# Kernel optimization log

Hardware: AMD Instinct MI355X
Metric: run time of the kernel (lower is better)

Reference implementation:

```python
import jax, jax.numpy as jnp
from jax import lax
import numpy as np

EPS = 1e-5

def _conv(x, w, pad):
    return lax.conv_general_dilated(x, w, (1, 1), ((pad, pad), (pad, pad)),
                                    dimension_numbers=('NCHW', 'OIHW', 'NCHW'))

def _bn_relu(x, g, b, m, v):
    scale = g * lax.rsqrt(v + EPS)
    shift = b - m * scale
    return jax.nn.relu(x * scale[:, None, None] + shift[:, None, None])

def _pam(x, kw, kb, vw, vb, gamma):
    # x: [B,C,H,W]; key/query share the same 1x1 conv (as in source)
    B, C, H, W = x.shape
    q = (_conv(x, kw, 0) + kb[:, None, None]).reshape(B, -1, H * W)      # [B,C/8,HW]
    attn = jax.nn.softmax(jnp.einsum('bci,bcj->bij', q, q), axis=-1)     # [B,HW,HW]
    v = (_conv(x, vw, 0) + vb[:, None, None]).reshape(B, C, H * W)       # [B,C,HW]
    out = jnp.einsum('bcj,bij->bci', v, attn).reshape(B, C, H, W)        # value @ attn^T
    return gamma * out + x

def _cam(x, gamma):
    B, C, H, W = x.shape
    f = x.reshape(B, C, H * W)
    energy = jnp.einsum('bcm,bdm->bcd', f, f)                            # [B,C,C]
    attn = jax.nn.softmax(jnp.max(energy, -1, keepdims=True) - energy, axis=-1)
    out = jnp.einsum('bcd,bdm->bcm', attn, f).reshape(B, C, H, W)
    return gamma * out + x

def setup_inputs() -> dict:
    key = jax.random.key(0)
    ks = iter(jax.random.split(key, 40))
    Cin, Cm, Cout = 512, 128, 64  # in_channels, in_channels//ratio, out_channels
    Ck = Cm // 8                  # PAM key channels
    n = lambda shape, s: jax.random.normal(next(ks), shape, jnp.float32) * s
    def bn(c):
        return dict(g=n((c,), 1.0) * 0 + 1.0 + n((c,), 0.1),
                    b=n((c,), 0.1), m=n((c,), 0.1), v=jnp.abs(n((c,), 0.5)) + 0.5)
    bn11, bn12, bn21, bn22 = bn(Cm), bn(Cm), bn(Cm), bn(Cm)
    return {
        'x': jax.random.normal(next(ks), (4, Cin, 64, 64), jnp.float32),
        'w11': n((Cm, Cin, 3, 3), 0.02), 'g11': bn11['g'], 'b11': bn11['b'], 'm11': bn11['m'], 'v11': bn11['v'],
        'w12': n((Cm, Cin, 3, 3), 0.02), 'g12': bn12['g'], 'b12': bn12['b'], 'm12': bn12['m'], 'v12': bn12['v'],
        'pam_kw': n((Ck, Cm, 1, 1), 0.05), 'pam_kb': n((Ck,), 0.02),
        'pam_vw': n((Cm, Cm, 1, 1), 0.05), 'pam_vb': n((Cm,), 0.02),
        'pam_gamma': n((1,), 0.1), 'cam_gamma': n((1,), 0.1),
        'w21': n((Cm, Cm, 3, 3), 0.03), 'g21': bn21['g'], 'b21': bn21['b'], 'm21': bn21['m'], 'v21': bn21['v'],
        'w22': n((Cm, Cm, 3, 3), 0.03), 'g22': bn22['g'], 'b22': bn22['b'], 'm22': bn22['m'], 'v22': bn22['v'],
        'w31': n((Cout, Cm, 1, 1), 0.05), 'b31': n((Cout,), 0.02),
        'w32': n((Cout, Cm, 1, 1), 0.05), 'b32': n((Cout,), 0.02),
        'w4':  n((Cout, Cm, 1, 1), 0.05), 'b4':  n((Cout,), 0.02),
    }

def reference(x, w11, g11, b11, m11, v11, w12, g12, b12, m12, v12,
              pam_kw, pam_kb, pam_vw, pam_vb, pam_gamma, cam_gamma,
              w21, g21, b21, m21, v21, w22, g22, b22, m22, v22,
              w31, b31, w32, b32, w4, b4):
    # Dropout2d(p=0.1) is identity at eval time; BatchNorm uses running stats.
    feat1 = _bn_relu(_conv(x, w11, 1), g11, b11, m11, v11)
    pa_feat = _pam(feat1, pam_kw, pam_kb, pam_vw, pam_vb, pam_gamma)
    pa_conv = _bn_relu(_conv(pa_feat, w21, 1), g21, b21, m21, v21)
    pa_out = _conv(pa_conv, w31, 0) + b31[:, None, None]

    feat2 = _bn_relu(_conv(x, w12, 1), g12, b12, m12, v12)
    ca_feat = _cam(feat2, cam_gamma)
    ca_conv = _bn_relu(_conv(ca_feat, w22, 1), g22, b22, m22, v22)
    ca_out = _conv(ca_conv, w32, 0) + b32[:, None, None]

    feat_sum = pa_conv + ca_conv
    feat_sum_out = _conv(feat_sum, w4, 0) + b4[:, None, None]
    return jnp.stack([pa_out, ca_out, feat_sum_out])  # [3,B,Cout,H,W]
```

## Files before the change

kernel.cpp:

```cpp
#include <hip/hip_runtime.h>
#include <stdint.h>

typedef unsigned short u16;
typedef unsigned int   u32;
typedef unsigned long long u64;
typedef __attribute__((ext_vector_type(8))) short bf16x8;
typedef __attribute__((ext_vector_type(4))) float f32x4;

#define DEV static __device__ __forceinline__

DEV float b2f(u16 u){ u32 x = ((u32)u) << 16; float f; __builtin_memcpy(&f, &x, 4); return f; }
DEV u16 f2b(float f){ u32 x; __builtin_memcpy(&x, &f, 4); return (u16)((x + 0x7fffu + ((x >> 16) & 1u)) >> 16); }
DEV float ldf(const void* p, int i, int flg){
  return flg ? b2f(((const u16*)p)[i]) : ((const float*)p)[i];
}
DEV void gload_lds16(const u16* g, u16* l){
  __builtin_amdgcn_global_load_lds((const __attribute__((address_space(1))) void*)g,
                                   (__attribute__((address_space(3))) void*)l, 16, 0, 0);
}

static constexpr int HW   = 4096;
static constexpr int PPIX = 4356;

__global__ void k_detect(const u32* __restrict__ x, int* __restrict__ flag)
{
  __shared__ int cnt;
  if (threadIdx.x == 0) cnt = 0;
  __syncthreads();
  const u32 w  = x[threadIdx.x];
  const u32 eb = (w >> 7) & 0xFFu;
  if (eb >= 100u && eb <= 150u) atomicAdd(&cnt, 1);
  __syncthreads();
  if (threadIdx.x == 0) *flag = (cnt > 384) ? 1 : 0;
}

__global__ void k_cvt(const void* __restrict__ src, const int* __restrict__ flagp,
                      u16* __restrict__ dst, int n)
{
  const int i = (blockIdx.x * 256 + threadIdx.x) << 2;
  if (i >= n) return;
  u64 ov;
  if (*flagp){
    ov = ((const u64*)src)[i >> 2];
  } else {
    const float4 f = ((const float4*)src)[i >> 2];
    const u16 a0 = f2b(f.x), a1 = f2b(f.y), a2 = f2b(f.z), a3 = f2b(f.w);
    ov = (u64)a0 | ((u64)a1 << 16) | ((u64)a2 << 32) | ((u64)a3 << 48);
  }
  ((u64*)dst)[i >> 2] = ov;
}

__global__ void k_prep(
    const void* g0,const void* b0,const void* m0,const void* v0,
    const void* g1,const void* b1,const void* m1,const void* v1,
    const void* g2,const void* b2,const void* m2,const void* v2,
    const void* g3,const void* b3,const void* m3,const void* v3,
    const int* __restrict__ flagp, float* scale, float* shift)
{
  const int t = threadIdx.x;
  if (t >= 512) return;
  const int flg = *flagp;
  const int set = t >> 7, c = t & 127;
  const void *gp,*bp,*mp,*vp;
  if      (set == 0){gp=g0;bp=b0;mp=m0;vp=v0;}
  else if (set == 1){gp=g1;bp=b1;mp=m1;vp=v1;}
  else if (set == 2){gp=g2;bp=b2;mp=m2;vp=v2;}
  else              {gp=g3;bp=b3;mp=m3;vp=v3;}
  const float sc = ldf(gp,c,flg) * rsqrtf(ldf(vp,c,flg) + 1e-5f);
  scale[t] = sc;
  shift[t] = ldf(bp,c,flg) - ldf(mp,c,flg) * sc;
}

__global__ void k_reorder_cvt(const void* __restrict__ win, const int* __restrict__ flagp,
                              u16* __restrict__ wout, int cin)
{
  const int idx = blockIdx.x * 256 + threadIdx.x;
  const int flg = *flagp;
  const int n9 = cin * 9;
  const int co = idx / n9;
  const int rem = idx - co * n9;
  const int ci = rem / 9;
  const int rs = rem - ci * 9;
  const u16 v = flg ? ((const u16*)win)[idx] : f2b(((const float*)win)[idx]);
  wout[co * n9 + rs * cin + ci] = v;
}

template<int C_>
__global__ void k_halo(u16* __restrict__ buf)
{
  const int tid = blockIdx.x * 256 + threadIdx.x;
  const int e  = tid * 8;
  const int cc = e % C_;
  int rem = e / C_;
  const int hp = rem % 260;
  const int b  = rem / 260;
  int pix;
  if      (hp < 66)  pix = hp;
  else if (hp < 132) pix = 65 * 66 + (hp - 66);
  else if (hp < 196) pix = (hp - 132 + 1) * 66;
  else               pix = (hp - 196 + 1) * 66 + 65;
  uint4 z; z.x = 0; z.y = 0; z.z = 0; z.w = 0;
  *(uint4*)(buf + ((size_t)b * PPIX + pix) * C_ + cc) = z;
}

__global__ __launch_bounds__(256) void k_xT(
    const void* __restrict__ src, const int* __restrict__ flagp, u16* __restrict__ dst)
{
  const int t = threadIdx.x, wave = t >> 6, lane = t & 63;
  const int pb = blockIdx.x & 31, ct = (blockIdx.x >> 5) & 7, b = blockIdx.x >> 8;
  const int c  = ct * 64 + lane;
  const int p0 = pb * 128 + wave * 32;
  const size_t sbase = ((size_t)(b * 512) + c) * 4096 + p0;

  u16 vals[32];
  if (*flagp){
    const u16* s = (const u16*)src + sbase;
    #pragma unroll
    for (int k = 0; k < 4; ++k){
      uint4 v = *(const uint4*)(s + k * 8);
      __builtin_memcpy(&vals[k * 8], &v, 16);
    }
  } else {
    const float* s = (const float*)src + sbase;
    #pragma unroll
    for (int k = 0; k < 8; ++k){
      float4 v = *(const float4*)(s + k * 4);
      vals[k*4+0] = f2b(v.x); vals[k*4+1] = f2b(v.y);
      vals[k*4+2] = f2b(v.z); vals[k*4+3] = f2b(v.w);
    }
  }
  const int hrow = (p0 >> 6) * 66 + (p0 & 63) + 67;
  u16* d = dst + ((size_t)b * PPIX + hrow) * 512 + c;
  #pragma unroll
  for (int k = 0; k < 32; ++k) d[(size_t)k * 512] = vals[k];
}

template<int CIN_, bool PADOUT_, bool DUALB_>
__global__ __launch_bounds__(256, 1) void k_cgemm(
    const u16* __restrict__ xA, const u16* __restrict__ xB,
    const u16* __restrict__ wA, const u16* __restrict__ wB,
    const float* __restrict__ scale, const float* __restrict__ shift,
    u16* __restrict__ outA, u16* __restrict__ outBp, u16* __restrict__ outB2)
{
  constexpr int K9   = 9 * CIN_;
  constexpr int NCH  = CIN_ / 64;
  constexpr int OPIX = PADOUT_ ? PPIX : 4096;

  __shared__ __align__(16) u16 At[128 * 64];
  __shared__ __align__(16) u16 Bt[128 * 64];

  const int t = threadIdx.x;
  const int w = t >> 6, lane = t & 63;
  const int l16 = lane & 15, quad = lane >> 4;

  const int cid = blockIdx.x >> 7;
  const int t7  = blockIdx.x & 127;
  const int b   = t7 >> 5;
  const int p0  = (t7 & 31) << 7;

  const u16* xin = cid ? xB : xA;
  const u16* wK  = cid ? wB : wA;
  const float* sc = scale + cid * 128;
  const float* sh = shift + cid * 128;

  const int rowS = t >> 3;
  const int sw   = ((t & 7) ^ (rowS & 7)) << 3;

  const u16* gA[4]; const u16* gB[4];
  u16* lA[4]; u16* lB[4];
  #pragma unroll
  for (int k = 0; k < 4; ++k){
    const int rA = k * 32 + rowS;
    gA[k] = wK + (size_t)rA * K9 + sw;
    const int px = p0 + k * 32 + rowS;
    const int h = px >> 6, wc = px & 63;
    gB[k] = xin + ((size_t)b * PPIX + h * 66 + wc) * CIN_ + sw;
    lA[k] = At + k * 2048 + w * 512;
    lB[k] = Bt + k * 2048 + w * 512;
  }

  f32x4 acc[4][4];
  #pragma unroll
  for (int mi = 0; mi < 4; ++mi)
    #pragma unroll
    for (int ni = 0; ni < 4; ++ni){
      acc[mi][ni][0]=0.f; acc[mi][ni][1]=0.f; acc[mi][ni][2]=0.f; acc[mi][ni][3]=0.f;
    }

  const int wc4 = (w >> 1) << 6;
  const int wp4 = (w & 1) << 6;

  #pragma unroll 1
  for (int tap = 0; tap < 9; ++tap){
    const int tb = (tap / 3) * 66 + (tap % 3);
    #pragma unroll 1
    for (int cc = 0; cc < NCH; ++cc){
      const int offA = tap * CIN_ + cc * 64;
      const int offB = tb  * CIN_ + cc * 64;
      #pragma unroll
      for (int k = 0; k < 4; ++k){
        gload_lds16(gA[k] + offA, lA[k]);
        gload_lds16(gB[k] + offB, lB[k]);
      }
      __syncthreads();
      #pragma unroll
      for (int ks = 0; ks < 2; ++ks){
        bf16x8 af[4], bf[4];
        const int col = ((ks * 4 + quad) ^ (l16 & 7)) << 3;
        #pragma unroll
        for (int mi = 0; mi < 4; ++mi)
          af[mi] = *(const bf16x8*)(At + ((wc4 + mi * 16 + l16) << 6) + col);
        #pragma unroll
        for (int ni = 0; ni < 4; ++ni)
          bf[ni] = *(const bf16x8*)(Bt + ((wp4 + ni * 16 + l16) << 6) + col);
        #pragma unroll
        for (int mi = 0; mi < 4; ++mi)
          #pragma unroll
          for (int ni = 0; ni < 4; ++ni)
            acc[mi][ni] = __builtin_amdgcn_mfma_f32_16x16x32_bf16(af[mi], bf[ni], acc[mi][ni], 0, 0, 0);
      }
      __syncthreads();
    }
  }

  u16* outp = cid ? outBp : outA;
  #pragma unroll
  for (int mi = 0; mi < 4; ++mi){
    #pragma unroll
    for (int ni = 0; ni < 4; ++ni){
      const int px = p0 + wp4 + ni * 16 + l16;
      const int opix = PADOUT_ ? ((px >> 6) * 66 + (px & 63) + 67) : px;
      const int co4 = wc4 + mi * 16 + quad * 4;
      u16 pk[4];
      #pragma unroll
      for (int rr = 0; rr < 4; ++rr)
        pk[rr] = f2b(fmaxf(acc[mi][ni][rr] * sc[co4 + rr] + sh[co4 + rr], 0.f));
      u64 pkv; __builtin_memcpy(&pkv, pk, 8);
      *(u64*)(outp + ((size_t)b * OPIX + opix) * 128 + co4) = pkv;
      if constexpr (DUALB_){
        if (cid){
          #pragma unroll
          for (int rr = 0; rr < 4; ++rr)
            outB2[((size_t)(b * 128) + co4 + rr) * 4096 + px] = pk[rr];
        }
      }
    }
  }
}

template<int CIN_, int CO_, int EPI_, bool SUM2_, bool PADIN_, bool PADOUT_, bool WPB_>
__global__ __launch_bounds__(256) void k_convT(
    const u16* __restrict__ xin, const u16* __restrict__ xin2,
    const u16* __restrict__ wK,
    const void* __restrict__ bias, const int* __restrict__ flagp,
    u16* __restrict__ outB, float* __restrict__ outF)
{
  constexpr int K    = CIN_;
  constexpr int MT   = CO_ / 16;
  constexpr int IPIX = PADIN_ ? PPIX : 4096;
  constexpr int OPIX = PADOUT_ ? PPIX : 4096;

  const int tid  = threadIdx.x;
  const int wave = tid >> 6;
  const int lane = tid & 63;
  const int l16  = lane & 15;
  const int quad = lane >> 4;

  int tile = blockIdx.x * 4 + wave;
  const int nt = tile & 255; tile >>= 8;
  const int mt = tile % MT;
  const int b  = tile / MT;

  const int p = nt * 16 + l16;
  const int h = p >> 6, wc = p & 63;

  const u16* wrow = wK + (WPB_ ? (size_t)b * CO_ * K : 0)
                       + (size_t)(mt * 16 + l16) * K + quad * 8;
  const u16* xb   = xin + (size_t)b * IPIX * CIN_ + quad * 8;

  f32x4 acc = {0.f, 0.f, 0.f, 0.f};

  const int poff = PADIN_ ? (h * 66 + wc + 67) : p;
  const u16* xrs = xb + (size_t)poff * CIN_;
  const u16* xrs2 = nullptr;
  if constexpr (SUM2_) xrs2 = xin2 + (size_t)b * IPIX * CIN_ + quad * 8 + (size_t)poff * CIN_;
  #pragma unroll
  for (int ci0 = 0; ci0 < CIN_; ci0 += 32){
    bf16x8 af = *(const bf16x8*)(wrow + ci0);
    bf16x8 bf;
    if constexpr (SUM2_){
      bf16x8 b1 = *(const bf16x8*)(xrs + ci0);
      bf16x8 b2 = *(const bf16x8*)(xrs2 + ci0);
      #pragma unroll
      for (int j = 0; j < 8; ++j)
        bf[j] = (short)f2b(b2f((u16)b1[j]) + b2f((u16)b2[j]));
    } else {
      bf = *(const bf16x8*)(xrs + ci0);
    }
    acc = __builtin_amdgcn_mfma_f32_16x16x32_bf16(af, bf, acc, 0, 0, 0);
  }

  const int flg = *flagp;

  if constexpr (EPI_ == 4){
    #pragma unroll
    for (int rr = 0; rr < 4; ++rr){
      const int co = quad * 4 + rr;
      const float vv = acc[rr] + ldf(bias, co, flg);
      const u16 hb = f2b(vv);
      const float lo = vv - b2f(hb);
      const size_t qaddr = ((size_t)b * 4096 + p) * 16 + co;
      outB[qaddr] = hb;
      ((u16*)outF)[qaddr] = f2b(lo);
    }
  } else if constexpr (EPI_ == 6){
    const float g = ldf(bias, 0, flg);
    const int opix = PADOUT_ ? (h * 66 + wc + 67) : p;
    const int co4 = mt * 16 + quad * 4;
    const size_t addr = ((size_t)b * OPIX + opix) * CO_ + co4;
    u64 rv = *(const u64*)(xin2 + (size_t)b * OPIX * CO_ + (size_t)opix * CO_ + co4);
    u16 rk[4]; __builtin_memcpy(rk, &rv, 8);
    u16 pk[4];
    #pragma unroll
    for (int rr = 0; rr < 4; ++rr)
      pk[rr] = f2b(g * acc[rr] + b2f(rk[rr]));
    u64 pkv; __builtin_memcpy(&pkv, pk, 8);
    *(u64*)(outB + addr) = pkv;
  } else {
    #pragma unroll
    for (int rr = 0; rr < 4; ++rr){
      const int co = mt * 16 + quad * 4 + rr;
      const float vv = acc[rr] + ldf(bias, co, flg);
      const size_t addr = ((size_t)(b * CO_) + co) * 4096 + p;
      if constexpr (EPI_ == 2) outB[addr] = f2b(vv);
      else { if (flg) outB[addr] = f2b(vv); else outF[addr] = vv; }
    }
  }
}

__global__ __launch_bounds__(256) void k_pam_flash(
    const u16* __restrict__ qTh, const u16* __restrict__ qTl,
    const u16* __restrict__ v,
    u16* __restrict__ po, float* __restrict__ pm, float* __restrict__ pl)
{
  __shared__ __align__(16) u16 vls[1024 * 8];
  __shared__ __align__(16) u16 pls[4][128 * 8];

  const int t    = threadIdx.x;
  const int wave = t >> 6, lane = t & 63;
  const int l16  = lane & 15, quad = lane >> 4;

  const int bid = blockIdx.x;
  const int js  = bid & 3, it = (bid >> 2) & 63, b = bid >> 8;
  const int i0  = it * 64;
  const int jbase = js * 1024;

  const u16* qTbh = qTh + ((size_t)b * 4096) * 16;
  const u16* qTbl = qTl + ((size_t)b * 4096) * 16;
  const u16* vb   = v + ((size_t)b * 128) * 4096;

  bf16x8 af_hl, af_h0 = {};
  {
    const int i = i0 + wave * 16 + l16;
    const u16* src = ((quad < 2) ? qTbh : qTbl) + (size_t)i * 16 + (quad & 1) * 8;
    *(uint4*)&af_hl = *(const uint4*)src;
    if (quad < 2) af_h0 = af_hl;
  }

  const u16* vsrcB[4];
  u16* vdstB[4];
  #pragma unroll
  for (int k = 0; k < 4; ++k){
    const int p = t + 256 * k;
    const int c  = ((p >> 7) << 4) | (p & 15);
    const int jl = ((p >> 6) & 1) * 32 + ((p >> 4) & 3) * 8;
    vsrcB[k] = vb + (size_t)c * 4096 + jbase + jl;
    vdstB[k] = vls + ((size_t)(wave * 64 + 256 * k)) * 8;
  }

  f32x4 oacc[8];
  #pragma unroll
  for (int cs = 0; cs < 8; ++cs){ oacc[cs][0]=0.f; oacc[cs][1]=0.f; oacc[cs][2]=0.f; oacc[cs][3]=0.f; }
  float m_run[4], l_run[4];
  #pragma unroll
  for (int r = 0; r < 4; ++r){ m_run[r] = -1e30f; l_run[r] = 0.f; }

  for (int ch = 0; ch < 16; ++ch){
    const int j0 = ch * 64;
    __syncthreads();
    #pragma unroll
    for (int k = 0; k < 4; ++k)
      gload_lds16(vsrcB[k] + j0, vdstB[k]);

    f32x4 sacc[4];
    #pragma unroll
    for (int ns = 0; ns < 4; ++ns){
      const int j = jbase + j0 + ns * 16 + l16;
      bf16x8 b_hh, b_ll;
      *(uint4*)&b_hh = *(const uint4*)(qTbh + (size_t)j * 16 + (quad & 1) * 8);
      *(uint4*)&b_ll = *(const uint4*)(qTbl + (size_t)j * 16 + (quad & 1) * 8);
      f32x4 z = {0.f, 0.f, 0.f, 0.f};
      z = __builtin_amdgcn_mfma_f32_16x16x32_bf16(af_hl, b_hh, z, 0, 0, 0);
      z = __builtin_amdgcn_mfma_f32_16x16x32_bf16(af_h0, b_ll, z, 0, 0, 0);
      sacc[ns] = z;
    }
    float pv[4][4];
    #pragma unroll
    for (int r = 0; r < 4; ++r){
      float mx = fmaxf(fmaxf(sacc[0][r], sacc[1][r]), fmaxf(sacc[2][r], sacc[3][r]));
      mx = fmaxf(mx, __shfl_xor(mx, 1));
      mx = fmaxf(mx, __shfl_xor(mx, 2));
      mx = fmaxf(mx, __shfl_xor(mx, 4));
      mx = fmaxf(mx, __shfl_xor(mx, 8));
      const float mnew  = fmaxf(m_run[r], mx);
      const float alpha = __expf(m_run[r] - mnew);
      m_run[r] = mnew;
      float rs = 0.f;
      #pragma unroll
      for (int ns = 0; ns < 4; ++ns){
        pv[ns][r] = __expf(sacc[ns][r] - mnew);
        rs += pv[ns][r];
      }
      rs += __shfl_xor(rs, 1); rs += __shfl_xor(rs, 2);
      rs += __shfl_xor(rs, 4); rs += __shfl_xor(rs, 8);
      l_run[r] = l_run[r] * alpha + rs;
      #pragma unroll
      for (int cs = 0; cs < 8; ++cs) oacc[cs][r] *= alpha;
    }
    #pragma unroll
    for (int ns = 0; ns < 4; ++ns){
      const int ks = ns >> 1;
      const int qp = (ns * 2 + (l16 >> 3)) & 3;
      #pragma unroll
      for (int r = 0; r < 4; ++r)
        pls[wave][(ks * 64 + qp * 16 + quad * 4 + r) * 8 + (l16 & 7)] = f2b(pv[ns][r]);
    }
    __syncthreads();
    #pragma unroll
    for (int ks = 0; ks < 2; ++ks){
      bf16x8 pf = *(const bf16x8*)(pls[wave] + ((ks * 64 + lane) << 3));
      #pragma unroll
      for (int cs = 0; cs < 8; ++cs){
        bf16x8 vf = *(const bf16x8*)(vls + (((cs * 2 + ks) * 64 + lane) << 3));
        oacc[cs] = __builtin_amdgcn_mfma_f32_16x16x32_bf16(pf, vf, oacc[cs], 0, 0, 0);
      }
    }
  }

  u16* pob = po + (size_t)bid * 64 * 128;
  #pragma unroll
  for (int cs = 0; cs < 8; ++cs)
    #pragma unroll
    for (int r = 0; r < 4; ++r)
      pob[(wave * 16 + quad * 4 + r) * 128 + cs * 16 + l16] = f2b(oacc[cs][r]);
  if (l16 == 0){
    #pragma unroll
    for (int r = 0; r < 4; ++r){
      pm[(size_t)bid * 64 + wave * 16 + quad * 4 + r] = m_run[r];
      pl[(size_t)bid * 64 + wave * 16 + quad * 4 + r] = l_run[r];
    }
  }
}

__global__ __launch_bounds__(256) void k_pam_comb2(
    const u16* __restrict__ po, const float* __restrict__ pm, const float* __restrict__ pl,
    const void* __restrict__ gptr, const int* __restrict__ flagp,
    u16* __restrict__ featT)
{
  __shared__ float wgt[4][64];
  const int t  = threadIdx.x;
  const int it = blockIdx.x & 63, b = blockIdx.x >> 6;
  const int base = (b * 64 + it) * 4;
  if (t < 64){
    const float m0 = pm[(size_t)(base+0)*64 + t];
    const float m1 = pm[(size_t)(base+1)*64 + t];
    const float m2 = pm[(size_t)(base+2)*64 + t];
    const float m3 = pm[(size_t)(base+3)*64 + t];
    const float M  = fmaxf(fmaxf(m0, m1), fmaxf(m2, m3));
    const float e0 = __expf(m0 - M), e1 = __expf(m1 - M);
    const float e2 = __expf(m2 - M), e3 = __expf(m3 - M);
    const float L  = pl[(size_t)(base+0)*64+t]*e0 + pl[(size_t)(base+1)*64+t]*e1
                   + pl[(size_t)(base+2)*64+t]*e2 + pl[(size_t)(base+3)*64+t]*e3;
    const float li = 1.0f / L;
    wgt[0][t] = e0*li; wgt[1][t] = e1*li; wgt[2][t] = e2*li; wgt[3][t] = e3*li;
  }
  __syncthreads();
  const float g = ldf(gptr, 0, *flagp);
  const int c = t & 127, ih = t >> 7;
  const int i0 = it * 64;
  for (int st = 0; st < 32; ++st){
    const int il = ih + st * 2;
    float acc = 0.f;
    #pragma unroll
    for (int s = 0; s < 4; ++s)
      acc += wgt[s][il] * b2f(po[((size_t)(base+s)*64 + il)*128 + c]);
    const int i = i0 + il;
    const int pix = (i >> 6) * 66 + (i & 63) + 67;
    u16* addr = featT + ((size_t)b * PPIX + pix) * 128 + c;
    *addr = f2b(g * acc + b2f(*addr));
  }
}

__global__ __launch_bounds__(128) void k_cam_attn(
    const u16* __restrict__ f, u16* __restrict__ attnc)
{
  __shared__ float fc[4096];
  __shared__ float red[128];
  const int d = threadIdx.x;
  const int c = blockIdx.x & 127, b = blockIdx.x >> 7;
  const u16* fb   = f + (size_t)b * 128 * HW;
  const u16* rowc = fb + (size_t)c * HW;
  for (int mi = d; mi < 4096; mi += 128) fc[mi] = b2f(rowc[mi]);
  __syncthreads();

  const u16* rowd = fb + (size_t)d * HW;
  float e = 0.f;
  for (int mm = 0; mm < 4096; mm += 8){
    const uint4 xv = *(const uint4*)(rowd + mm);
    const u16* px = (const u16*)&xv;
    #pragma unroll
    for (int k = 0; k < 8; ++k) e += fc[mm + k] * b2f(px[k]);
  }
  red[d] = e;
  __syncthreads();
  for (int st = 64; st > 0; st >>= 1){
    if (d < st) red[d] = fminf(red[d], red[d + st]);
    __syncthreads();
  }
  const float emin = red[0];
  __syncthreads();
  const float pd = __expf(emin - e);
  red[d] = pd;
  __syncthreads();
  for (int st = 64; st > 0; st >>= 1){
    if (d < st) red[d] += red[d + st];
    __syncthreads();
  }
  attnc[((size_t)b * 128 + c) * 128 + d] = f2b(pd / red[0]);
}

extern "C" void kernel_launch(void* const* d_in, const int* in_sizes, int n_in,
                              void* d_out, int out_size, void* d_ws, size_t ws_size,
                              hipStream_t stream)
{
  (void)in_sizes; (void)n_in; (void)out_size; (void)ws_size;

  const void* x    = d_in[0];
  const void* w11  = d_in[1];
  const void* g11  = d_in[2];
  const void* b11  = d_in[3];
  const void* m11  = d_in[4];
  const void* v11  = d_in[5];
  const void* w12  = d_in[6];
  const void* g12  = d_in[7];
  const void* b12  = d_in[8];
  const void* m12  = d_in[9];
  const void* v12  = d_in[10];
  const void* kw   = d_in[11];
  const void* kb   = d_in[12];
  const void* vw   = d_in[13];
  const void* vb   = d_in[14];
  const void* pgam = d_in[15];
  const void* cgam = d_in[16];
  const void* w21  = d_in[17];
  const void* g21  = d_in[18];
  const void* b21  = d_in[19];
  const void* m21  = d_in[20];
  const void* v21  = d_in[21];
  const void* w22  = d_in[22];
  const void* g22  = d_in[23];
  const void* b22  = d_in[24];
  const void* m22  = d_in[25];
  const void* v22  = d_in[26];
  const void* w31  = d_in[27];
  const void* b31  = d_in[28];
  const void* w32  = d_in[29];
  const void* b32  = d_in[30];
  const void* w4   = d_in[31];
  const void* b4   = d_in[32];

  char* wsb = (char*)d_ws;
  size_t off = 0;
  auto alloc = [&](size_t bytes) -> void* {
    void* pp = wsb + off;
    off += (bytes + 255) & ~(size_t)255;
    return pp;
  };
  u16*   xT      = (u16*)alloc((size_t)4 * PPIX * 512 * 2);
  u16*   feat1T  = (u16*)alloc((size_t)4 * PPIX * 128 * 2);
  u16*   feat2T  = (u16*)alloc((size_t)4 * PPIX * 128 * 2);
  u16*   feat2cm = (u16*)alloc((size_t)4 * 128 * HW * 2);
  u16*   cafeatT = (u16*)alloc((size_t)4 * PPIX * 128 * 2);
  u16*   vbuf    = (u16*)alloc((size_t)4 * 128 * HW * 2);
  u16*   caconvT = (u16*)alloc((size_t)4 * HW * 128 * 2);
  u16*   qTh     = (u16*)alloc((size_t)4 * HW * 16 * 2);
  u16*   qTl     = (u16*)alloc((size_t)4 * HW * 16 * 2);
  float* pm      = (float*)alloc((size_t)1024 * 64 * 4);
  float* pl      = (float*)alloc((size_t)1024 * 64 * 4);
  u16*   attnc   = (u16*)alloc((size_t)4 * 128 * 128 * 2);
  float* scale   = (float*)alloc(512 * 4);
  float* shift   = (float*)alloc(512 * 4);
  u16*   w11r    = (u16*)alloc((size_t)128 * 4608 * 2);
  u16*   w12r    = (u16*)alloc((size_t)128 * 4608 * 2);
  u16*   w21r    = (u16*)alloc((size_t)128 * 1152 * 2);
  u16*   w22r    = (u16*)alloc((size_t)128 * 1152 * 2);
  u16*   kwb     = (u16*)alloc((size_t)16 * 128 * 2);
  u16*   vwb     = (u16*)alloc((size_t)128 * 128 * 2);
  u16*   w31b    = (u16*)alloc((size_t)64 * 128 * 2);
  u16*   w32b    = (u16*)alloc((size_t)64 * 128 * 2);
  u16*   w4b     = (u16*)alloc((size_t)64 * 128 * 2);
  int*   flag    = (int*)alloc(256);
  u16*   po      = xT;

  k_detect<<<1, 512, 0, stream>>>((const u32*)x, flag);
  k_prep<<<1, 512, 0, stream>>>(g11,b11,m11,v11, g12,b12,m12,v12,
                                g21,b21,m21,v21, g22,b22,m22,v22, flag, scale, shift);
  k_halo<512><<<260, 256, 0, stream>>>(xT);
  k_halo<128><<<65, 256, 0, stream>>>(feat1T);
  k_halo<128><<<65, 256, 0, stream>>>(cafeatT);
  k_xT<<<1024, 256, 0, stream>>>(x, flag, xT);
  k_reorder_cvt<<<2304, 256, 0, stream>>>(w11, flag, w11r, 512);
  k_reorder_cvt<<<2304, 256, 0, stream>>>(w12, flag, w12r, 512);
  k_reorder_cvt<<<576, 256, 0, stream>>>(w21, flag, w21r, 128);
  k_reorder_cvt<<<576, 256, 0, stream>>>(w22, flag, w22r, 128);
  k_cvt<<<2, 256, 0, stream>>>(kw, flag, kwb, 16 * 128);
  k_cvt<<<16, 256, 0, stream>>>(vw, flag, vwb, 128 * 128);
  k_cvt<<<8, 256, 0, stream>>>(w31, flag, w31b, 64 * 128);
  k_cvt<<<8, 256, 0, stream>>>(w32, flag, w32b, 64 * 128);
  k_cvt<<<8, 256, 0, stream>>>(w4, flag, w4b, 64 * 128);

  k_cgemm<512, true, true><<<256, 256, 0, stream>>>(
      xT, xT, w11r, w12r, scale, shift, feat1T, feat2T, feat2cm);

  k_convT<128,16,4,false,true,false,false><<<256,256,0,stream>>>(
      feat1T, nullptr, kwb, kb, flag, qTh, (float*)qTl);
  k_convT<128,128,2,false,true,false,false><<<2048,256,0,stream>>>(
      feat1T, nullptr, vwb, vb, flag, vbuf, nullptr);
  k_pam_flash<<<1024, 256, 0, stream>>>(qTh, qTl, vbuf, po, pm, pl);
  k_pam_comb2<<<256, 256, 0, stream>>>(po, pm, pl, pgam, flag, feat1T);

  k_cam_attn<<<512, 128, 0, stream>>>(feat2cm, attnc);
  k_convT<128,128,6,false,true,true,true><<<2048,256,0,stream>>>(
      feat2T, feat2T, attnc, cgam, flag, cafeatT, nullptr);

  k_cgemm<128, false, false><<<256, 256, 0, stream>>>(
      feat1T, cafeatT, w21r, w22r, scale + 256, shift + 256, vbuf, caconvT, nullptr);

  const size_t SEC = (size_t)4 * 64 * HW;
  u16*   outB = (u16*)d_out;
  float* outF = (float*)d_out;
  k_convT<128,64,3,false,false,false,false><<<1024,256,0,stream>>>(
      vbuf,    nullptr, w31b, b31, flag, outB,           outF);
  k_convT<128,64,3,false,false,false,false><<<1024,256,0,stream>>>(
      caconvT, nullptr, w32b, b32, flag, outB + SEC,     outF + SEC);
  k_convT<128,64,3,true ,false,false,false><<<1024,256,0,stream>>>(
      vbuf,    caconvT, w4b,  b4,  flag, outB + 2 * SEC, outF + 2 * SEC);
}
```

Before: 480.2 us.

## Merge prep launches, precompute PAM row max, MFMA-based CAM energy

Merges the detect, convert, reorder and halo kernels into fewer launches so fewer small kernels are dispatched. In PAM flash attention, a first pass computes the exact row max from the high-half scores, so the online-softmax rescaling, shuffles and running-sum reduction go away; row sums are now accumulated with an extra MFMA against a ones vector. CAM energy moves from a scalar per-row dot-product kernel to an MFMA tile kernel with far fewer blocks. The row max is approximated from the high part only and probabilities are truncated to bf16, which may shift numerics slightly, and the extra max pass adds Q reads.

```diff
diff --git a/kernel.cpp b/kernel.cpp
--- a/kernel.cpp
+++ b/kernel.cpp
@@ -11,6 +11,7 @@
 
 DEV float b2f(u16 u){ u32 x = ((u32)u) << 16; float f; __builtin_memcpy(&f, &x, 4); return f; }
 DEV u16 f2b(float f){ u32 x; __builtin_memcpy(&x, &f, 4); return (u16)((x + 0x7fffu + ((x >> 16) & 1u)) >> 16); }
+DEV u16 f2b_trunc(float f){ u32 x; __builtin_memcpy(&x, &f, 4); return (u16)(x >> 16); }
 DEV float ldf(const void* p, int i, int flg){
   return flg ? b2f(((const u16*)p)[i]) : ((const float*)p)[i];
 }
@@ -22,44 +23,26 @@
 static constexpr int HW   = 4096;
 static constexpr int PPIX = 4356;
 
-__global__ void k_detect(const u32* __restrict__ x, int* __restrict__ flag)
-{
-  __shared__ int cnt;
-  if (threadIdx.x == 0) cnt = 0;
-  __syncthreads();
-  const u32 w  = x[threadIdx.x];
-  const u32 eb = (w >> 7) & 0xFFu;
-  if (eb >= 100u && eb <= 150u) atomicAdd(&cnt, 1);
-  __syncthreads();
-  if (threadIdx.x == 0) *flag = (cnt > 384) ? 1 : 0;
-}
-
-__global__ void k_cvt(const void* __restrict__ src, const int* __restrict__ flagp,
-                      u16* __restrict__ dst, int n)
-{
-  const int i = (blockIdx.x * 256 + threadIdx.x) << 2;
-  if (i >= n) return;
-  u64 ov;
-  if (*flagp){
-    ov = ((const u64*)src)[i >> 2];
-  } else {
-    const float4 f = ((const float4*)src)[i >> 2];
-    const u16 a0 = f2b(f.x), a1 = f2b(f.y), a2 = f2b(f.z), a3 = f2b(f.w);
-    ov = (u64)a0 | ((u64)a1 << 16) | ((u64)a2 << 32) | ((u64)a3 << 48);
-  }
-  ((u64*)dst)[i >> 2] = ov;
-}
-
 __global__ void k_prep(
+    const u32* __restrict__ x,
     const void* g0,const void* b0,const void* m0,const void* v0,
     const void* g1,const void* b1,const void* m1,const void* v1,
     const void* g2,const void* b2,const void* m2,const void* v2,
     const void* g3,const void* b3,const void* m3,const void* v3,
-    const int* __restrict__ flagp, float* scale, float* shift)
-{
+    int* __restrict__ flag, float* scale, float* shift)
+{
+  __shared__ int cnt;
+  __shared__ int sflag;
   const int t = threadIdx.x;
-  if (t >= 512) return;
-  const int flg = *flagp;
+  if (t == 0) cnt = 0;
+  __syncthreads();
+  const u32 w  = x[t];
+  const u32 eb = (w >> 7) & 0xFFu;
+  if (eb >= 100u && eb <= 150u) atomicAdd(&cnt, 1);
+  __syncthreads();
+  if (t == 0){ sflag = (cnt > 384) ? 1 : 0; *flag = sflag; }
+  __syncthreads();
+  const int flg = sflag;
   const int set = t >> 7, c = t & 127;
   const void *gp,*bp,*mp,*vp;
   if      (set == 0){gp=g0;bp=b0;mp=m0;vp=v0;}
@@ -71,10 +54,43 @@
   shift[t] = ldf(bp,c,flg) - ldf(mp,c,flg) * sc;
 }
 
-__global__ void k_reorder_cvt(const void* __restrict__ win, const int* __restrict__ flagp,
-                              u16* __restrict__ wout, int cin)
-{
-  const int idx = blockIdx.x * 256 + threadIdx.x;
+__global__ void k_cvt5(
+    const void* s0,const void* s1,const void* s2,const void* s3,const void* s4,
+    const int* __restrict__ flagp,
+    u16* d0,u16* d1,u16* d2,u16* d3,u16* d4)
+{
+  const int g = blockIdx.x * 256 + threadIdx.x;
+  if (g >= 10752) return;
+  const void* s; u16* d; int base;
+  if      (g < 512) { s=s0; d=d0; base=0;    }
+  else if (g < 4608){ s=s1; d=d1; base=512;  }
+  else if (g < 6656){ s=s2; d=d2; base=4608; }
+  else if (g < 8704){ s=s3; d=d3; base=6656; }
+  else              { s=s4; d=d4; base=8704; }
+  const int i = g - base;
+  u64 ov;
+  if (*flagp){
+    ov = ((const u64*)s)[i];
+  } else {
+    const float4 f = ((const float4*)s)[i];
+    const u16 a0 = f2b(f.x), a1 = f2b(f.y), a2 = f2b(f.z), a3 = f2b(f.w);
+    ov = (u64)a0 | ((u64)a1 << 16) | ((u64)a2 << 32) | ((u64)a3 << 48);
+  }
+  ((u64*)d)[i] = ov;
+}
+
+__global__ void k_reorder4(
+    const void* w11,const void* w12,const void* w21,const void* w22,
+    const int* __restrict__ flagp,
+    u16* o11,u16* o12,u16* o21,u16* o22)
+{
+  int blk = blockIdx.x;
+  const void* win; u16* wout; int cin;
+  if      (blk < 2304){ win=w11; wout=o11; cin=512; }
+  else if (blk < 4608){ win=w12; wout=o12; cin=512; blk-=2304; }
+  else if (blk < 5184){ win=w21; wout=o21; cin=128; blk-=4608; }
+  else                { win=w22; wout=o22; cin=128; blk-=5184; }
+  const int idx = blk * 256 + threadIdx.x;
   const int flg = *flagp;
   const int n9 = cin * 9;
   const int co = idx / n9;
@@ -85,13 +101,17 @@
   wout[co * n9 + rs * cin + ci] = v;
 }
 
-template<int C_>
-__global__ void k_halo(u16* __restrict__ buf)
-{
-  const int tid = blockIdx.x * 256 + threadIdx.x;
+__global__ void k_halo3(u16* __restrict__ xT, u16* __restrict__ f1, u16* __restrict__ cf)
+{
+  int blk = blockIdx.x;
+  u16* buf; int cmask, csh;
+  if      (blk < 260){ buf = xT; cmask = 511; csh = 9; }
+  else if (blk < 325){ buf = f1; cmask = 127; csh = 7; blk -= 260; }
+  else               { buf = cf; cmask = 127; csh = 7; blk -= 325; }
+  const int tid = blk * 256 + threadIdx.x;
   const int e  = tid * 8;
-  const int cc = e % C_;
-  int rem = e / C_;
+  const int cc = e & cmask;
+  const int rem = e >> csh;
   const int hp = rem % 260;
   const int b  = rem / 260;
   int pix;
@@ -100,7 +120,7 @@
   else if (hp < 196) pix = (hp - 132 + 1) * 66;
   else               pix = (hp - 196 + 1) * 66 + 65;
   uint4 z; z.x = 0; z.y = 0; z.z = 0; z.w = 0;
-  *(uint4*)(buf + ((size_t)b * PPIX + pix) * C_ + cc) = z;
+  *(uint4*)(buf + ((size_t)b * PPIX + pix) * (cmask + 1) + cc) = z;
 }
 
 __global__ __launch_bounds__(256) void k_xT(
@@ -367,6 +387,31 @@
     if (quad < 2) af_h0 = af_hl;
   }
 
+  float mloc[4] = {-3e38f, -3e38f, -3e38f, -3e38f};
+  #pragma unroll 1
+  for (int ch = 0; ch < 16; ++ch){
+    #pragma unroll
+    for (int ns = 0; ns < 4; ++ns){
+      const int j = jbase + ch * 64 + ns * 16 + l16;
+      bf16x8 bh;
+      *(uint4*)&bh = *(const uint4*)(qTbh + (size_t)j * 16 + (quad & 1) * 8);
+      f32x4 z = {0.f, 0.f, 0.f, 0.f};
+      z = __builtin_amdgcn_mfma_f32_16x16x32_bf16(af_hl, bh, z, 0, 0, 0);
+      #pragma unroll
+      for (int r = 0; r < 4; ++r) mloc[r] = fmaxf(mloc[r], z[r]);
+    }
+  }
+  float mrow[4];
+  #pragma unroll
+  for (int r = 0; r < 4; ++r){
+    float mm = mloc[r];
+    mm = fmaxf(mm, __shfl_xor(mm, 1));
+    mm = fmaxf(mm, __shfl_xor(mm, 2));
+    mm = fmaxf(mm, __shfl_xor(mm, 4));
+    mm = fmaxf(mm, __shfl_xor(mm, 8));
+    mrow[r] = mm;
+  }
+
   const u16* vsrcB[4];
   u16* vdstB[4];
   #pragma unroll
@@ -378,13 +423,15 @@
     vdstB[k] = vls + ((size_t)(wave * 64 + 256 * k)) * 8;
   }
 
+  const short oneb = (short)0x3F80;
+  const bf16x8 vones = {oneb,oneb,oneb,oneb,oneb,oneb,oneb,oneb};
+
   f32x4 oacc[8];
   #pragma unroll
   for (int cs = 0; cs < 8; ++cs){ oacc[cs][0]=0.f; oacc[cs][1]=0.f; oacc[cs][2]=0.f; oacc[cs][3]=0.f; }
-  float m_run[4], l_run[4];
-  #pragma unroll
-  for (int r = 0; r < 4; ++r){ m_run[r] = -1e30f; l_run[r] = 0.f; }
-
+  f32x4 lacc = {0.f, 0.f, 0.f, 0.f};
+
+  #pragma unroll 1
   for (int ch = 0; ch < 16; ++ch){
     const int j0 = ch * 64;
     __syncthreads();
@@ -392,48 +439,22 @@
     for (int k = 0; k < 4; ++k)
       gload_lds16(vsrcB[k] + j0, vdstB[k]);
 
-    f32x4 sacc[4];
     #pragma unroll
     for (int ns = 0; ns < 4; ++ns){
       const int j = jbase + j0 + ns * 16 + l16;
-      bf16x8 b_hh, b_ll;
-      *(uint4*)&b_hh = *(const uint4*)(qTbh + (size_t)j * 16 + (quad & 1) * 8);
-      *(uint4*)&b_ll = *(const uint4*)(qTbl + (size_t)j * 16 + (quad & 1) * 8);
+      bf16x8 bh, bl;
+      *(uint4*)&bh = *(const uint4*)(qTbh + (size_t)j * 16 + (quad & 1) * 8);
+      *(uint4*)&bl = *(const uint4*)(qTbl + (size_t)j * 16 + (quad & 1) * 8);
       f32x4 z = {0.f, 0.f, 0.f, 0.f};
-      z = __builtin_amdgcn_mfma_f32_16x16x32_bf16(af_hl, b_hh, z, 0, 0, 0);
-      z = __builtin_amdgcn_mfma_f32_16x16x32_bf16(af_h0, b_ll, z, 0, 0, 0);
-      sacc[ns] = z;
-    }
-    float pv[4][4];
-    #pragma unroll
-    for (int r = 0; r < 4; ++r){
-      float mx = fmaxf(fmaxf(sacc[0][r], sacc[1][r]), fmaxf(sacc[2][r], sacc[3][r]));
-      mx = fmaxf(mx, __shfl_xor(mx, 1));
-      mx = fmaxf(mx, __shfl_xor(mx, 2));
-      mx = fmaxf(mx, __shfl_xor(mx, 4));
-      mx = fmaxf(mx, __shfl_xor(mx, 8));
-      const float mnew  = fmaxf(m_run[r], mx);
-      const float alpha = __expf(m_run[r] - mnew);
-      m_run[r] = mnew;
-      float rs = 0.f;
-      #pragma unroll
-      for (int ns = 0; ns < 4; ++ns){
-        pv[ns][r] = __expf(sacc[ns][r] - mnew);
-        rs += pv[ns][r];
-      }
-      rs += __shfl_xor(rs, 1); rs += __shfl_xor(rs, 2);
-      rs += __shfl_xor(rs, 4); rs += __shfl_xor(rs, 8);
-      l_run[r] = l_run[r] * alpha + rs;
-      #pragma unroll
-      for (int cs = 0; cs < 8; ++cs) oacc[cs][r] *= alpha;
-    }
-    #pragma unroll
-    for (int ns = 0; ns < 4; ++ns){
+      z = __builtin_amdgcn_mfma_f32_16x16x32_bf16(af_hl, bh, z, 0, 0, 0);
+      z = __builtin_amdgcn_mfma_f32_16x16x32_bf16(af_h0, bl, z, 0, 0, 0);
       const int ks = ns >> 1;
       const int qp = (ns * 2 + (l16 >> 3)) & 3;
       #pragma unroll
-      for (int r = 0; r < 4; ++r)
-        pls[wave][(ks * 64 + qp * 16 + quad * 4 + r) * 8 + (l16 & 7)] = f2b(pv[ns][r]);
+      for (int r = 0; r < 4; ++r){
+        const float p = __expf(z[r] - mrow[r]);
+        pls[wave][(ks * 64 + qp * 16 + quad * 4 + r) * 8 + (l16 & 7)] = f2b_trunc(p);
+      }
     }
     __syncthreads();
     #pragma unroll
@@ -444,6 +465,7 @@
         bf16x8 vf = *(const bf16x8*)(vls + (((cs * 2 + ks) * 64 + lane) << 3));
         oacc[cs] = __builtin_amdgcn_mfma_f32_16x16x32_bf16(pf, vf, oacc[cs], 0, 0, 0);
       }
+      lacc = __builtin_amdgcn_mfma_f32_16x16x32_bf16(pf, vones, lacc, 0, 0, 0);
     }
   }
 
@@ -456,8 +478,8 @@
   if (l16 == 0){
     #pragma unroll
     for (int r = 0; r < 4; ++r){
-      pm[(size_t)bid * 64 + wave * 16 + quad * 4 + r] = m_run[r];
-      pl[(size_t)bid * 64 + wave * 16 + quad * 4 + r] = l_run[r];
+      pm[(size_t)bid * 64 + wave * 16 + quad * 4 + r] = mrow[r];
+      pl[(size_t)bid * 64 + wave * 16 + quad * 4 + r] = lacc[r];
     }
   }
 }
@@ -501,42 +523,51 @@
   }
 }
 
-__global__ __launch_bounds__(128) void k_cam_attn(
+__global__ __launch_bounds__(256) void k_cam_energy(
     const u16* __restrict__ f, u16* __restrict__ attnc)
 {
-  __shared__ float fc[4096];
-  __shared__ float red[128];
-  const int d = threadIdx.x;
-  const int c = blockIdx.x & 127, b = blockIdx.x >> 7;
-  const u16* fb   = f + (size_t)b * 128 * HW;
-  const u16* rowc = fb + (size_t)c * HW;
-  for (int mi = d; mi < 4096; mi += 128) fc[mi] = b2f(rowc[mi]);
+  __shared__ float els[16][132];
+  const int t = threadIdx.x, wave = t >> 6, lane = t & 63;
+  const int l16 = lane & 15, quad = lane >> 4;
+  const int ct = blockIdx.x & 7, b = blockIdx.x >> 3;
+  const u16* fb = f + (size_t)b * 128 * 4096;
+  const int c0 = ct * 16;
+  const int d0 = wave * 32;
+
+  f32x4 e0 = {0.f,0.f,0.f,0.f}, e1 = {0.f,0.f,0.f,0.f};
+  #pragma unroll 2
+  for (int k0 = 0; k0 < 4096; k0 += 32){
+    bf16x8 afr, bf0, bf1;
+    *(uint4*)&afr = *(const uint4*)(fb + (size_t)(c0 + l16) * 4096 + k0 + quad * 8);
+    *(uint4*)&bf0 = *(const uint4*)(fb + (size_t)(d0 + l16) * 4096 + k0 + quad * 8);
+    *(uint4*)&bf1 = *(const uint4*)(fb + (size_t)(d0 + 16 + l16) * 4096 + k0 + quad * 8);
+    e0 = __builtin_amdgcn_mfma_f32_16x16x32_bf16(afr, bf0, e0, 0, 0, 0);
+    e1 = __builtin_amdgcn_mfma_f32_16x16x32_bf16(afr, bf1, e1, 0, 0, 0);
+  }
+  #pragma unroll
+  for (int r = 0; r < 4; ++r){
+    els[quad * 4 + r][d0 + l16]      = e0[r];
+    els[quad * 4 + r][d0 + 16 + l16] = e1[r];
+  }
   __syncthreads();
-
-  const u16* rowd = fb + (size_t)d * HW;
-  float e = 0.f;
-  for (int mm = 0; mm < 4096; mm += 8){
-    const uint4 xv = *(const uint4*)(rowd + mm);
-    const u16* px = (const u16*)&xv;
-    #pragma unroll
-    for (int k = 0; k < 8; ++k) e += fc[mm + k] * b2f(px[k]);
-  }
-  red[d] = e;
-  __syncthreads();
-  for (int st = 64; st > 0; st >>= 1){
-    if (d < st) red[d] = fminf(red[d], red[d + st]);
-    __syncthreads();
-  }
-  const float emin = red[0];
-  __syncthreads();
-  const float pd = __expf(emin - e);
-  red[d] = pd;
-  __syncthreads();
-  for (int st = 64; st > 0; st >>= 1){
-    if (d < st) red[d] += red[d + st];
-    __syncthreads();
-  }
-  attnc[((size_t)b * 128 + c) * 128 + d] = f2b(pd / red[0]);
+  const int c = wave * 4 + quad, sg = l16;
+  float mn = 3e38f;
+  float ev[8];
+  #pragma unroll
+  for (int k = 0; k < 8; ++k){ ev[k] = els[c][sg * 8 + k]; mn = fminf(mn, ev[k]); }
+  mn = fminf(mn, __shfl_xor(mn, 1));
+  mn = fminf(mn, __shfl_xor(mn, 2));
+  mn = fminf(mn, __shfl_xor(mn, 4));
+  mn = fminf(mn, __shfl_xor(mn, 8));
+  float s = 0.f;
+  #pragma unroll
+  for (int k = 0; k < 8; ++k){ ev[k] = __expf(mn - ev[k]); s += ev[k]; }
+  s += __shfl_xor(s, 1); s += __shfl_xor(s, 2);
+  s += __shfl_xor(s, 4); s += __shfl_xor(s, 8);
+  const float inv = 1.0f / s;
+  u16* dst = attnc + ((size_t)b * 128 + c0 + c) * 128 + sg * 8;
+  #pragma unroll
+  for (int k = 0; k < 8; ++k) dst[k] = f2b(ev[k] * inv);
 }
 
 extern "C" void kernel_launch(void* const* d_in, const int* in_sizes, int n_in,
@@ -612,22 +643,13 @@
   int*   flag    = (int*)alloc(256);
   u16*   po      = xT;
 
-  k_detect<<<1, 512, 0, stream>>>((const u32*)x, flag);
-  k_prep<<<1, 512, 0, stream>>>(g11,b11,m11,v11, g12,b12,m12,v12,
+  k_prep<<<1, 512, 0, stream>>>((const u32*)x,
+                                g11,b11,m11,v11, g12,b12,m12,v12,
                                 g21,b21,m21,v21, g22,b22,m22,v22, flag, scale, shift);
-  k_halo<512><<<260, 256, 0, stream>>>(xT);
-  k_halo<128><<<65, 256, 0, stream>>>(feat1T);
-  k_halo<128><<<65, 256, 0, stream>>>(cafeatT);
+  k_halo3<<<390, 256, 0, stream>>>(xT, feat1T, cafeatT);
   k_xT<<<1024, 256, 0, stream>>>(x, flag, xT);
-  k_reorder_cvt<<<2304, 256, 0, stream>>>(w11, flag, w11r, 512);
-  k_reorder_cvt<<<2304, 256, 0, stream>>>(w12, flag, w12r, 512);
-  k_reorder_cvt<<<576, 256, 0, stream>>>(w21, flag, w21r, 128);
-  k_reorder_cvt<<<576, 256, 0, stream>>>(w22, flag, w22r, 128);
-  k_cvt<<<2, 256, 0, stream>>>(kw, flag, kwb, 16 * 128);
-  k_cvt<<<16, 256, 0, stream>>>(vw, flag, vwb, 128 * 128);
-  k_cvt<<<8, 256, 0, stream>>>(w31, flag, w31b, 64 * 128);
-  k_cvt<<<8, 256, 0, stream>>>(w32, flag, w32b, 64 * 128);
-  k_cvt<<<8, 256, 0, stream>>>(w4, flag, w4b, 64 * 128);
+  k_reorder4<<<5760, 256, 0, stream>>>(w11, w12, w21, w22, flag, w11r, w12r, w21r, w22r);
+  k_cvt5<<<42, 256, 0, stream>>>(kw, vw, w31, w32, w4, flag, kwb, vwb, w31b, w32b, w4b);
 
   k_cgemm<512, true, true><<<256, 256, 0, stream>>>(
       xT, xT, w11r, w12r, scale, shift, feat1T, feat2T, feat2cm);
@@ -639,7 +661,7 @@
   k_pam_flash<<<1024, 256, 0, stream>>>(qTh, qTl, vbuf, po, pm, pl);
   k_pam_comb2<<<256, 256, 0, stream>>>(po, pm, pl, pgam, flag, feat1T);
 
-  k_cam_attn<<<512, 128, 0, stream>>>(feat2cm, attnc);
+  k_cam_energy<<<32, 256, 0, stream>>>(feat2cm, attnc);
   k_convT<128,128,6,false,true,true,true><<<2048,256,0,stream>>>(
       feat2T, feat2T, attnc, cgam, flag, cafeatT, nullptr);
 
```

Result: faster. 420.3 us (-12.5%).
